# Optimization experiments

Measured on AMD Instinct MI355X. Metric: run time of the kernel, lower is better.

The kernel has to match this reference:

```python
import jax, jax.numpy as jnp
import numpy as np

B, C, N, V, W = 2, 32, 4, 32, 32
E = 256          # spa_dim
H = 8            # num_heads
D = E // H       # head_dim
K_H, K_W = 7, 7  # mask_field
EPS = 1e-5


def layer_norm(x, g, b):
    mu = jnp.mean(x, axis=-1, keepdims=True)
    var = jnp.mean(jnp.square(x - mu), axis=-1, keepdims=True)
    return (x - mu) * jax.lax.rsqrt(var + EPS) * g + b


def local_window_mask(h, w, k_h, k_w):
    # boolean [h*w, h*w]: query (i,j) attends keys (p,q) with p in [i-k_h//2, i+k_h-k_h//2), q likewise
    lh, rh = k_h // 2, k_h - k_h // 2
    lw, rw = k_w // 2, k_w - k_w // 2
    di = jnp.arange(h)[None, :] - jnp.arange(h)[:, None]   # [h(query), h(key)] = p - i
    dj = jnp.arange(w)[None, :] - jnp.arange(w)[:, None]
    mh = (di >= -lh) & (di < rh)
    mw = (dj >= -lw) & (dj < rw)
    m = mh[:, None, :, None] & mw[None, :, None, :]        # [h, w, h, w]
    return m.reshape(h * w, h * w)


def setup_inputs() -> dict:
    key = jax.random.key(0)
    ks = jax.random.split(key, 13)
    s = 0.02
    return {
        "x_lf": jax.random.normal(ks[0], (B, C, N, V, W), jnp.float32),
        "x_hf": jax.random.normal(ks[1], (B, C, N, V, W), jnp.float32),
        "w_in": jax.random.normal(ks[2], (E, C), jnp.float32) * s,       # linear_in.weight [out,in]
        "w_qk": jax.random.normal(ks[3], (E, C), jnp.float32) * s,       # linear_qk.weight
        "ln_g": jnp.ones((E,), jnp.float32),
        "ln_b": jnp.zeros((E,), jnp.float32),
        "in_proj_w": jax.random.normal(ks[4], (3 * E, E), jnp.float32) * s,
        "out_proj_w": jax.random.normal(ks[5], (E, E), jnp.float32) * s,
        "ln2_g": jnp.ones((E,), jnp.float32),
        "ln2_b": jnp.zeros((E,), jnp.float32),
        "ff_w1": jax.random.normal(ks[6], (2 * E, E), jnp.float32) * s,
        "ff_w2": jax.random.normal(ks[7], (E, 2 * E), jnp.float32) * s,
        "w_out": jax.random.normal(ks[8], (C, E), jnp.float32) * s,
    }


def reference(x_lf, x_hf, w_in, w_qk, ln_g, ln_b, in_proj_w, out_proj_w,
              ln2_g, ln2_b, ff_w1, ff_w2, w_out):
    b, c, n, v, w = x_lf.shape
    L, Bn = v * w, b * n
    mask = local_window_mask(v, w, K_H, K_W)                      # [L, L] bool

    # 'b c n v w -> (v w) (b n) c'
    tok = jnp.transpose(x_lf, (3, 4, 0, 2, 1)).reshape(L, Bn, c)
    kv = jnp.transpose(x_hf, (3, 4, 0, 2, 1)).reshape(L, Bn, c)

    epi_token = tok @ w_in.T                                       # [L, Bn, E]
    epi_kv = kv @ w_qk.T
    q_in = layer_norm(epi_token, ln_g, ln_b)
    k_in = layer_norm(epi_kv, ln_g, ln_b)
    v_in = epi_kv                                                  # value is un-normalized epi_kv

    wq, wk, wv = in_proj_w[:E], in_proj_w[E:2 * E], in_proj_w[2 * E:]
    def heads(x, wgt):
        y = x @ wgt.T                                              # [L, Bn, E]
        return jnp.transpose(y.reshape(L, Bn, H, D), (1, 2, 0, 3)) # [Bn, H, L, D]
    Q, K, Vv = heads(q_in, wq), heads(k_in, wk), heads(v_in, wv)

    scores = jnp.einsum('bhqd,bhkd->bhqk', Q, K) / jnp.sqrt(jnp.float32(D))
    scores = jnp.where(mask[None, None], scores, -jnp.inf)
    attn = jax.nn.softmax(scores, axis=-1)
    ctx = jnp.einsum('bhqk,bhkd->bhqd', attn, Vv)                  # [Bn, H, L, D]
    ctx = jnp.transpose(ctx, (2, 0, 1, 3)).reshape(L, Bn, E)
    epi_token = ctx @ out_proj_w.T + epi_token

    ff = layer_norm(epi_token, ln2_g, ln2_b)
    ff = jax.nn.relu(ff @ ff_w1.T) @ ff_w2.T
    epi_token = ff + epi_token

    out = epi_token @ w_out.T                                      # [L, Bn, C]
    # '(v w) (b n) c -> b c n v w'
    return jnp.transpose(out.reshape(v, w, b, n, c), (2, 4, 3, 0, 1))
```

## Files before the change

### kernel.cpp

```cpp
#include <hip/hip_runtime.h>
#include <hip/hip_bf16.h>


typedef __attribute__((ext_vector_type(8))) short short8v;
typedef __attribute__((ext_vector_type(4))) float f32x4;

__device__ __forceinline__ unsigned short f2bf(float x) {
    union { float f; unsigned u; } c; c.f = x;
    unsigned r = c.u + 0x7FFFu + ((c.u >> 16) & 1u);
    return (unsigned short)(r >> 16);
}
__device__ __forceinline__ float bf2f(short b) {
    union { unsigned u; float f; } c;
    c.u = ((unsigned)(unsigned short)b) << 16;
    return c.f;
}

__global__ __launch_bounds__(512) void embed_conv_kernel(
    const float* __restrict__ x_lf, const float* __restrict__ x_hf,
    const float* __restrict__ w_in, const float* __restrict__ w_qk,
    const float* __restrict__ ln_g, const float* __restrict__ ln_b,
    unsigned short* __restrict__ epi_b, unsigned short* __restrict__ kv_b,
    unsigned short* __restrict__ q_b, unsigned short* __restrict__ k_b,
    const float* __restrict__ wqkv, const float* __restrict__ wop,
    const float* __restrict__ wff1, const float* __restrict__ wff2,
    unsigned short* __restrict__ o1, unsigned short* __restrict__ o2,
    unsigned short* __restrict__ o3, unsigned short* __restrict__ o4)
{
    __shared__ float xs[2][32][36];
    __shared__ float part[2][2][2][4][4][2];

    int tid = threadIdx.x;
    int m0 = blockIdx.x * 32;
    int bn = m0 >> 10, l0 = m0 & 1023;
    int bb = bn >> 2, nn = bn & 3;

    {
        int t = tid >> 8, rem = tid & 255;
        int c = rem >> 3, i0 = (rem & 7) * 4;
        size_t base = (size_t)bb * 131072 + (size_t)c * 4096 + nn * 1024 + l0 + i0;
        const float* src = t ? x_hf : x_lf;
        *(float4*)&xs[t][c][i0] = *(const float4*)(src + base);
    }
    __syncthreads();

    int lane = tid & 63, wv = tid >> 6;
    int rA = lane & 15, k8r = lane >> 4, g = k8r, k0 = k8r * 8;
    int p = wv >> 2, rg = (wv >> 1) & 1, chh = wv & 1;
    const float* W = p ? w_qk : w_in;

    short8v afrag;
#pragma unroll
    for (int j = 0; j < 8; ++j)
        afrag[j] = (short)f2bf(xs[p][k0 + j][rg * 16 + rA]);

    f32x4 acc[8];
#pragma unroll
    for (int ct = 0; ct < 8; ++ct)
#pragma unroll
        for (int r = 0; r < 4; ++r) acc[ct][r] = 0.f;

#pragma unroll
    for (int ct = 0; ct < 8; ++ct) {
        const float* wp = W + ((chh * 8 + ct) * 16 + rA) * 32 + k0;
        float4 w0 = *(const float4*)wp;
        float4 w1 = *(const float4*)(wp + 4);
        short8v bfrag;
        bfrag[0] = (short)f2bf(w0.x); bfrag[1] = (short)f2bf(w0.y);
        bfrag[2] = (short)f2bf(w0.z); bfrag[3] = (short)f2bf(w0.w);
        bfrag[4] = (short)f2bf(w1.x); bfrag[5] = (short)f2bf(w1.y);
        bfrag[6] = (short)f2bf(w1.z); bfrag[7] = (short)f2bf(w1.w);
        acc[ct] = __builtin_amdgcn_mfma_f32_16x16x32_bf16(afrag, bfrag, acc[ct], 0, 0, 0);
    }

    float s[4] = {0.f, 0.f, 0.f, 0.f}, q[4] = {0.f, 0.f, 0.f, 0.f};
#pragma unroll
    for (int ct = 0; ct < 8; ++ct)
#pragma unroll
        for (int r = 0; r < 4; ++r) {
            float v = acc[ct][r];
            s[r] += v; q[r] += v * v;
        }
#pragma unroll
    for (int off = 8; off; off >>= 1)
#pragma unroll
        for (int r = 0; r < 4; ++r) {
            s[r] += __shfl_xor(s[r], off);
            q[r] += __shfl_xor(q[r], off);
        }
    if (rA == 0) {
#pragma unroll
        for (int r = 0; r < 4; ++r) {
            part[p][rg][chh][g][r][0] = s[r];
            part[p][rg][chh][g][r][1] = q[r];
        }
    }
    __syncthreads();
    float mu[4], rs[4];
#pragma unroll
    for (int r = 0; r < 4; ++r) {
        float S = part[p][rg][0][g][r][0] + part[p][rg][1][g][r][0];
        float Q = part[p][rg][0][g][r][1] + part[p][rg][1][g][r][1];
        mu[r] = S * (1.f / 256.f);
        rs[r] = rsqrtf(Q * (1.f / 256.f) - mu[r] * mu[r] + 1e-5f);
    }

#pragma unroll
    for (int ct = 0; ct < 8; ++ct) {
        int col = (chh * 8 + ct) * 16 + rA;
        float gg = ln_g[col], bv = ln_b[col];
#pragma unroll
        for (int r = 0; r < 4; ++r) {
            int row = m0 + rg * 16 + g * 4 + r;
            float v = acc[ct][r];
            float lnv = (v - mu[r]) * rs[r] * gg + bv;
            size_t o = (size_t)row * 256 + col;
            if (p == 0) {
                epi_b[o] = f2bf(v);
                q_b[o] = f2bf(lnv);
            } else {
                kv_b[o] = f2bf(v);
                k_b[o] = f2bf(lnv);
            }
        }
    }

    {
        int i4 = blockIdx.x * 512 + tid;
        const float* src; unsigned short* dst; int off;
        if (i4 < 49152)      { src = wqkv; dst = o1; off = i4 * 4; }
        else if (i4 < 65536) { src = wop;  dst = o2; off = (i4 - 49152) * 4; }
        else if (i4 < 98304) { src = wff1; dst = o3; off = (i4 - 65536) * 4; }
        else                 { src = wff2; dst = o4; off = (i4 - 98304) * 4; }
        float4 v = *(const float4*)(src + off);
        ushort4 u;
        u.x = f2bf(v.x); u.y = f2bf(v.y); u.z = f2bf(v.z); u.w = f2bf(v.w);
        *(ushort4*)(dst + off) = u;
    }
}

template <int OUTMAP, bool RELU>
__global__ __launch_bounds__(256) void gemm_mfma64(
    const unsigned short* __restrict__ A0, const unsigned short* __restrict__ A1,
    const unsigned short* __restrict__ A2, const unsigned short* __restrict__ Wb,
    unsigned short* __restrict__ OUT, int K, int N)
{
    int z = blockIdx.z;
    const unsigned short* A = (z == 0) ? A0 : (z == 1) ? A1 : A2;
    const unsigned short* W = Wb + (size_t)z * 65536;

    __shared__ unsigned short As[64 * 72];
    __shared__ unsigned short Ws[128 * 72];

    int tid = threadIdx.x;
    int lane = tid & 63, wid = tid >> 6;
    int wm = wid >> 1, wn = wid & 1;
    int m0 = blockIdx.x * 64, n0 = blockIdx.y * 128;

    f32x4 acc[2][4];
#pragma unroll
    for (int i = 0; i < 2; ++i)
#pragma unroll
        for (int j = 0; j < 4; ++j)
#pragma unroll
            for (int r = 0; r < 4; ++r) acc[i][j][r] = 0.f;

    int rA = lane & 15, k8r = lane >> 4, g = lane >> 4;

    for (int kc = 0; kc < K; kc += 64) {
#pragma unroll
        for (int t = 0; t < 2; ++t) {
            int idx = t * 256 + tid;
            int row = idx >> 3, k8 = idx & 7;
            *(short8v*)&As[row * 72 + k8 * 8] =
                *(const short8v*)(A + (size_t)(m0 + row) * K + kc + k8 * 8);
        }
#pragma unroll
        for (int t = 0; t < 4; ++t) {
            int idx = t * 256 + tid;
            int row = idx >> 3, k8 = idx & 7;
            *(short8v*)&Ws[row * 72 + k8 * 8] =
                *(const short8v*)(W + (size_t)(n0 + row) * K + kc + k8 * 8);
        }
        __syncthreads();

        short8v a[2][2], b[2][4];
#pragma unroll
        for (int ks = 0; ks < 2; ++ks) {
#pragma unroll
            for (int mi = 0; mi < 2; ++mi)
                a[ks][mi] = *(const short8v*)&As[(wm * 32 + mi * 16 + rA) * 72 + ks * 32 + k8r * 8];
#pragma unroll
            for (int ni = 0; ni < 4; ++ni)
                b[ks][ni] = *(const short8v*)&Ws[(wn * 64 + ni * 16 + rA) * 72 + ks * 32 + k8r * 8];
        }
#pragma unroll
        for (int ks = 0; ks < 2; ++ks)
#pragma unroll
            for (int mi = 0; mi < 2; ++mi)
#pragma unroll
                for (int ni = 0; ni < 4; ++ni)
                    acc[mi][ni] = __builtin_amdgcn_mfma_f32_16x16x32_bf16(
                        a[ks][mi], b[ks][ni], acc[mi][ni], 0, 0, 0);
        __syncthreads();
    }

#pragma unroll
    for (int mi = 0; mi < 2; ++mi) {
#pragma unroll
        for (int ni = 0; ni < 4; ++ni) {
#pragma unroll
            for (int r = 0; r < 4; ++r) {
                int row = m0 + wm * 32 + mi * 16 + g * 4 + r;
                int col = n0 + wn * 64 + ni * 16 + rA;
                float v = acc[mi][ni][r];
                if (RELU) v = fmaxf(v, 0.f);
                if (OUTMAP == 0) {
                    OUT[(size_t)row * N + col] = f2bf(v);
                } else {
                    int l = row & 1023, bn = row >> 10;
                    int h = col >> 5, d = col & 31;
                    OUT[(size_t)z * 2097152 + ((bn * 8 + h) * 1024 + l) * 32 + d] = f2bf(v);
                }
            }
        }
    }
}

__global__ __launch_bounds__(256) void attn_mfma_kernel(
    const unsigned short* __restrict__ Qb, const unsigned short* __restrict__ Kb,
    const unsigned short* __restrict__ Vb, unsigned short* __restrict__ ctx)
{
    int bh = blockIdx.x >> 5;
    int qv = blockIdx.x & 31;
    int tid = threadIdx.x, lane = tid & 63, wv = tid >> 6;
    int rA = lane & 15, k8r = lane >> 4, g = lane >> 4;

    __shared__ unsigned short KPs[7 * 32 * 40];
    __shared__ unsigned short Vt[32 * 232];
    __shared__ float redm[2][2][4][4];
    __shared__ float reds[2][2][4][4];

    unsigned short* Ks = KPs;
    unsigned short* Ps = KPs;

    int mt = wv & 1, nh = wv >> 1;

    short8v qfrag = *(const short8v*)(
        Qb + ((size_t)bh * 1024 + qv * 32 + mt * 16 + rA) * 32 + k8r * 8);

#pragma unroll
    for (int it = 0; it < 4; ++it) {
        int idx = it * 256 + tid;
        if (idx < 896) {
            int dv = idx >> 7, rem = idx & 127;
            int kw = rem >> 2, c8 = (rem & 3) * 8;
            int kvc = min(max(qv - 3 + dv, 0), 31);
            size_t base = ((size_t)bh * 1024 + kvc * 32 + kw) * 32 + c8;
            int n = dv * 32 + kw;
            *(short8v*)&Ks[n * 40 + c8] = *(const short8v*)(Kb + base);
            short8v v8 = *(const short8v*)(Vb + base);
#pragma unroll
            for (int j = 0; j < 8; ++j)
                Vt[(c8 + j) * 232 + n] = (unsigned short)v8[j];
        }
    }
    __syncthreads();

    f32x4 sc[7];
#pragma unroll
    for (int ct = 0; ct < 7; ++ct)
#pragma unroll
        for (int r = 0; r < 4; ++r) sc[ct][r] = 0.f;
#pragma unroll
    for (int ct = 0; ct < 7; ++ct) {
        short8v b = *(const short8v*)&Ks[(nh * 112 + ct * 16 + rA) * 40 + k8r * 8];
        sc[ct] = __builtin_amdgcn_mfma_f32_16x16x32_bf16(qfrag, b, sc[ct], 0, 0, 0);
    }

    const float scale = 0.17677669529663687f;
    float mx[4] = {-1e30f, -1e30f, -1e30f, -1e30f};
#pragma unroll
    for (int ct = 0; ct < 7; ++ct) {
        int n = nh * 112 + ct * 16 + rA;
        int dv = n >> 5, kw = n & 31;
        int kv = qv - 3 + dv;
        bool vv = (kv >= 0) && (kv < 32);
#pragma unroll
        for (int r = 0; r < 4; ++r) {
            int qw = mt * 16 + g * 4 + r;
            int dj = kw - qw;
            bool ok = vv && (dj >= -3) && (dj <= 3);
            float s = ok ? sc[ct][r] * scale : -1e30f;
            sc[ct][r] = s;
            mx[r] = fmaxf(mx[r], s);
        }
    }
#pragma unroll
    for (int off = 8; off; off >>= 1)
#pragma unroll
        for (int r = 0; r < 4; ++r) mx[r] = fmaxf(mx[r], __shfl_xor(mx[r], off));
    if (rA == 0) {
#pragma unroll
        for (int r = 0; r < 4; ++r) redm[mt][nh][g][r] = mx[r];
    }
    __syncthreads();
#pragma unroll
    for (int r = 0; r < 4; ++r)
        mx[r] = fmaxf(redm[mt][0][g][r], redm[mt][1][g][r]);

    float sm[4] = {0.f, 0.f, 0.f, 0.f};
#pragma unroll
    for (int ct = 0; ct < 7; ++ct)
#pragma unroll
        for (int r = 0; r < 4; ++r) {
            float e = __expf(sc[ct][r] - mx[r]);
            sc[ct][r] = e;
            sm[r] += e;
        }
#pragma unroll
    for (int off = 8; off; off >>= 1)
#pragma unroll
        for (int r = 0; r < 4; ++r) sm[r] += __shfl_xor(sm[r], off);
    if (rA == 0) {
#pragma unroll
        for (int r = 0; r < 4; ++r) reds[mt][nh][g][r] = sm[r];
    }
    __syncthreads();
    float inv[4];
#pragma unroll
    for (int r = 0; r < 4; ++r)
        inv[r] = 1.f / (reds[mt][0][g][r] + reds[mt][1][g][r]);

#pragma unroll
    for (int ct = 0; ct < 7; ++ct) {
        int n = nh * 112 + ct * 16 + rA;
#pragma unroll
        for (int r = 0; r < 4; ++r) {
            int q = mt * 16 + g * 4 + r;
            Ps[q * 232 + n] = f2bf(sc[ct][r]);
        }
    }
    __syncthreads();

    f32x4 o;
#pragma unroll
    for (int r = 0; r < 4; ++r) o[r] = 0.f;
#pragma unroll
    for (int kb = 0; kb < 7; ++kb) {
        short8v pa = *(const short8v*)&Ps[(mt * 16 + rA) * 232 + kb * 32 + k8r * 8];
        short8v vb = *(const short8v*)&Vt[(nh * 16 + rA) * 232 + kb * 32 + k8r * 8];
        o = __builtin_amdgcn_mfma_f32_16x16x32_bf16(pa, vb, o, 0, 0, 0);
    }

    {
        int bn = bh >> 3, h = bh & 7;
        int d = nh * 16 + rA;
#pragma unroll
        for (int r = 0; r < 4; ++r) {
            int q = qv * 32 + mt * 16 + g * 4 + r;
            ctx[((size_t)bn * 1024 + q) * 256 + h * 32 + d] = f2bf(o[r] * inv[r]);
        }
    }
}

__global__ __launch_bounds__(512) void outproj_ln_kernel(
    const unsigned short* __restrict__ ctx, const unsigned short* __restrict__ Wop,
    unsigned short* __restrict__ epi_b, const float* __restrict__ g2,
    const float* __restrict__ b2, unsigned short* __restrict__ ffin)
{
    __shared__ unsigned short As[32 * 72];
    __shared__ unsigned short Ws[256 * 72];
    __shared__ float part[2][4][4][4][2];

    int tid = threadIdx.x, lane = tid & 63, wv = tid >> 6;
    int m0 = blockIdx.x * 32;
    int rA = lane & 15, k8r = lane >> 4, g = lane >> 4;
    int rg = wv & 1, ch = wv >> 1;

    f32x4 acc[4];
#pragma unroll
    for (int ct = 0; ct < 4; ++ct)
#pragma unroll
        for (int r = 0; r < 4; ++r) acc[ct][r] = 0.f;

    for (int kc = 0; kc < 256; kc += 64) {
        if (tid < 256) {
            int row = tid >> 3, k8 = tid & 7;
            *(short8v*)&As[row * 72 + k8 * 8] =
                *(const short8v*)(ctx + (size_t)(m0 + row) * 256 + kc + k8 * 8);
        }
#pragma unroll
        for (int t = 0; t < 4; ++t) {
            int idx = t * 512 + tid;
            int row = idx >> 3, k8 = idx & 7;
            *(short8v*)&Ws[row * 72 + k8 * 8] =
                *(const short8v*)(Wop + (size_t)row * 256 + kc + k8 * 8);
        }
        __syncthreads();
        short8v a[2];
#pragma unroll
        for (int ks = 0; ks < 2; ++ks)
            a[ks] = *(const short8v*)&As[(rg * 16 + rA) * 72 + ks * 32 + k8r * 8];
#pragma unroll
        for (int ks = 0; ks < 2; ++ks)
#pragma unroll
            for (int ct = 0; ct < 4; ++ct) {
                short8v b = *(const short8v*)&Ws[(ch * 64 + ct * 16 + rA) * 72 + ks * 32 + k8r * 8];
                acc[ct] = __builtin_amdgcn_mfma_f32_16x16x32_bf16(a[ks], b, acc[ct], 0, 0, 0);
            }
        __syncthreads();
    }

    float s[4] = {0.f, 0.f, 0.f, 0.f}, q[4] = {0.f, 0.f, 0.f, 0.f};
#pragma unroll
    for (int ct = 0; ct < 4; ++ct) {
        int col = ch * 64 + ct * 16 + rA;
#pragma unroll
        for (int r = 0; r < 4; ++r) {
            int row = m0 + rg * 16 + g * 4 + r;
            float v = acc[ct][r] + bf2f(epi_b[(size_t)row * 256 + col]);
            acc[ct][r] = v;
            s[r] += v; q[r] += v * v;
        }
    }
#pragma unroll
    for (int off = 8; off; off >>= 1)
#pragma unroll
        for (int r = 0; r < 4; ++r) {
            s[r] += __shfl_xor(s[r], off);
            q[r] += __shfl_xor(q[r], off);
        }
    if (rA == 0) {
#pragma unroll
        for (int r = 0; r < 4; ++r) {
            part[rg][ch][g][r][0] = s[r];
            part[rg][ch][g][r][1] = q[r];
        }
    }
    __syncthreads();
    float mu[4], rs[4];
#pragma unroll
    for (int r = 0; r < 4; ++r) {
        float S = part[rg][0][g][r][0] + part[rg][1][g][r][0]
                + part[rg][2][g][r][0] + part[rg][3][g][r][0];
        float Q = part[rg][0][g][r][1] + part[rg][1][g][r][1]
                + part[rg][2][g][r][1] + part[rg][3][g][r][1];
        mu[r] = S * (1.f / 256.f);
        rs[r] = rsqrtf(Q * (1.f / 256.f) - mu[r] * mu[r] + 1e-5f);
    }
#pragma unroll
    for (int ct = 0; ct < 4; ++ct) {
        int col = ch * 64 + ct * 16 + rA;
        float gg = g2[col], bv = b2[col];
#pragma unroll
        for (int r = 0; r < 4; ++r) {
            int row = m0 + rg * 16 + g * 4 + r;
            size_t o = (size_t)row * 256 + col;
            epi_b[o] = f2bf(acc[ct][r]);
            ffin[o] = f2bf((acc[ct][r] - mu[r]) * rs[r] * gg + bv);
        }
    }
}

__global__ __launch_bounds__(512) void ff2_final_kernel(
    const unsigned short* __restrict__ ffh, const unsigned short* __restrict__ W2,
    const unsigned short* __restrict__ epi_b, const float* __restrict__ w_out,
    float* __restrict__ out)
{
    __shared__ unsigned short As[32 * 72];
    __shared__ unsigned short Ws[256 * 72];
    __shared__ unsigned short Ts[32 * 264];

    int tid = threadIdx.x, lane = tid & 63, wv = tid >> 6;
    int m0 = blockIdx.x * 32;
    int rA = lane & 15, k8r = lane >> 4, g = lane >> 4;
    int rg = wv & 1, ch = wv >> 1;

    f32x4 acc[4];
#pragma unroll
    for (int ct = 0; ct < 4; ++ct)
#pragma unroll
        for (int r = 0; r < 4; ++r) acc[ct][r] = 0.f;

    for (int kc = 0; kc < 512; kc += 64) {
        if (tid < 256) {
            int row = tid >> 3, k8 = tid & 7;
            *(short8v*)&As[row * 72 + k8 * 8] =
                *(const short8v*)(ffh + (size_t)(m0 + row) * 512 + kc + k8 * 8);
        }
#pragma unroll
        for (int t = 0; t < 4; ++t) {
            int idx = t * 512 + tid;
            int row = idx >> 3, k8 = idx & 7;
            *(short8v*)&Ws[row * 72 + k8 * 8] =
                *(const short8v*)(W2 + (size_t)row * 512 + kc + k8 * 8);
        }
        __syncthreads();
        short8v a[2];
#pragma unroll
        for (int ks = 0; ks < 2; ++ks)
            a[ks] = *(const short8v*)&As[(rg * 16 + rA) * 72 + ks * 32 + k8r * 8];
#pragma unroll
        for (int ks = 0; ks < 2; ++ks)
#pragma unroll
            for (int ct = 0; ct < 4; ++ct) {
                short8v b = *(const short8v*)&Ws[(ch * 64 + ct * 16 + rA) * 72 + ks * 32 + k8r * 8];
                acc[ct] = __builtin_amdgcn_mfma_f32_16x16x32_bf16(a[ks], b, acc[ct], 0, 0, 0);
            }
        __syncthreads();
    }

#pragma unroll
    for (int ct = 0; ct < 4; ++ct) {
        int col = ch * 64 + ct * 16 + rA;
#pragma unroll
        for (int r = 0; r < 4; ++r) {
            int lrow = rg * 16 + g * 4 + r;
            float v = acc[ct][r] + bf2f(epi_b[(size_t)(m0 + lrow) * 256 + col]);
            Ts[lrow * 264 + col] = f2bf(v);
        }
    }
    __syncthreads();

    int bn = m0 >> 10, l0 = m0 & 1023;
    int bb = bn >> 2, nn = bn & 3;

    if (wv < 4) {
        int rw = wv & 1, cw = wv >> 1;
        f32x4 a2;
#pragma unroll
        for (int r = 0; r < 4; ++r) a2[r] = 0.f;
#pragma unroll
        for (int ks = 0; ks < 8; ++ks) {
            short8v af = *(const short8v*)&Ts[(rw * 16 + rA) * 264 + ks * 32 + k8r * 8];
            const float* wp = w_out + (cw * 16 + rA) * 256 + ks * 32 + k8r * 8;
            float4 w0 = *(const float4*)wp;
            float4 w1 = *(const float4*)(wp + 4);
            short8v bf;
            bf[0] = (short)f2bf(w0.x); bf[1] = (short)f2bf(w0.y);
            bf[2] = (short)f2bf(w0.z); bf[3] = (short)f2bf(w0.w);
            bf[4] = (short)f2bf(w1.x); bf[5] = (short)f2bf(w1.y);
            bf[6] = (short)f2bf(w1.z); bf[7] = (short)f2bf(w1.w);
            a2 = __builtin_amdgcn_mfma_f32_16x16x32_bf16(af, bf, a2, 0, 0, 0);
        }
        int c = cw * 16 + rA;
        int l = l0 + rw * 16 + g * 4;
        float4 st; st.x = a2[0]; st.y = a2[1]; st.z = a2[2]; st.w = a2[3];
        *(float4*)(out + ((size_t)(bb * 32 + c) * 4 + nn) * 1024 + l) = st;
    }
}

extern "C" void kernel_launch(void* const* d_in, const int* in_sizes, int n_in,
                              void* d_out, int out_size, void* d_ws, size_t ws_size,
                              hipStream_t stream) {
    const float* x_lf       = (const float*)d_in[0];
    const float* x_hf       = (const float*)d_in[1];
    const float* w_in       = (const float*)d_in[2];
    const float* w_qk       = (const float*)d_in[3];
    const float* ln_g       = (const float*)d_in[4];
    const float* ln_b       = (const float*)d_in[5];
    const float* in_proj_w  = (const float*)d_in[6];
    const float* out_proj_w = (const float*)d_in[7];
    const float* ln2_g      = (const float*)d_in[8];
    const float* ln2_b      = (const float*)d_in[9];
    const float* ff_w1      = (const float*)d_in[10];
    const float* ff_w2      = (const float*)d_in[11];
    const float* w_out      = (const float*)d_in[12];
    float* out = (float*)d_out;

    char* w = (char*)d_ws;
    unsigned short* epi_b  = (unsigned short*)(w);
    unsigned short* Qb     = (unsigned short*)(w + (4u  << 20));
    unsigned short* Kb     = (unsigned short*)(w + (8u  << 20));
    unsigned short* Vb     = (unsigned short*)(w + (12u << 20));
    unsigned short* q_b    = (unsigned short*)(w + (16u << 20));
    unsigned short* k_b    = (unsigned short*)(w + (20u << 20));
    unsigned short* kv_b   = (unsigned short*)(w + (24u << 20));
    unsigned short* ctx_b  = (unsigned short*)(w + (28u << 20));
    unsigned short* ffin_b = (unsigned short*)(w + (32u << 20));
    unsigned short* ffh_b  = (unsigned short*)(w + (36u << 20));
    unsigned short* wqkv_b = (unsigned short*)(w + (44u << 20));
    unsigned short* wop_b  = (unsigned short*)(w + (45u << 20));
    unsigned short* wff1_b = (unsigned short*)(w + (46u << 20));
    unsigned short* wff2_b = (unsigned short*)(w + (47u << 20));

    embed_conv_kernel<<<256, 512, 0, stream>>>(
        x_lf, x_hf, w_in, w_qk, ln_g, ln_b, epi_b, kv_b, q_b, k_b,
        in_proj_w, out_proj_w, ff_w1, ff_w2, wqkv_b, wop_b, wff1_b, wff2_b);
    gemm_mfma64<1, false><<<dim3(128, 2, 3), 256, 0, stream>>>(
        q_b, k_b, kv_b, wqkv_b, Qb, 256, 256);
    attn_mfma_kernel<<<2048, 256, 0, stream>>>(Qb, Kb, Vb, ctx_b);
    outproj_ln_kernel<<<256, 512, 0, stream>>>(ctx_b, wop_b, epi_b,
                                               ln2_g, ln2_b, ffin_b);
    gemm_mfma64<0, true><<<dim3(128, 4, 1), 256, 0, stream>>>(
        ffin_b, ffin_b, ffin_b, wff1_b, ffh_b, 256, 512);
    ff2_final_kernel<<<256, 512, 0, stream>>>(ffh_b, wff2_b, epi_b, w_out, out);
}
```

Before: 73.57 us.

## Process two query rows per attention block and drop cross-wave softmax reductions

Each attention block now handles two adjacent query rows (64 queries) sharing an 8-row key/value window of 256 keys, so the grid is halved. Each wave owns 16 full query rows across all 256 keys, which lets the softmax max and sum be done with lane shuffles only and removes the shared-memory reduction barriers. The cost is more masked MFMA work per query (256 keys instead of 224) and a larger per-thread score array, which may raise register pressure.

```diff
diff --git a/kernel.cpp b/kernel.cpp
--- a/kernel.cpp
+++ b/kernel.cpp
@@ -231,66 +231,66 @@
     const unsigned short* __restrict__ Qb, const unsigned short* __restrict__ Kb,
     const unsigned short* __restrict__ Vb, unsigned short* __restrict__ ctx)
 {
-    int bh = blockIdx.x >> 5;
-    int qv = blockIdx.x & 31;
-    int tid = threadIdx.x, lane = tid & 63, wv = tid >> 6;
+    int bh = blockIdx.x >> 4;
+    int qv0 = (blockIdx.x & 15) * 2;
+    int tid = threadIdx.x, lane = tid & 63, mt = tid >> 6;
     int rA = lane & 15, k8r = lane >> 4, g = lane >> 4;
 
-    __shared__ unsigned short KPs[7 * 32 * 40];
-    __shared__ unsigned short Vt[32 * 232];
-    __shared__ float redm[2][2][4][4];
-    __shared__ float reds[2][2][4][4];
+    __shared__ unsigned short KPs[64 * 264];
+    __shared__ unsigned short Vt[32 * 264];
 
     unsigned short* Ks = KPs;
     unsigned short* Ps = KPs;
 
-    int mt = wv & 1, nh = wv >> 1;
-
-    short8v qfrag = *(const short8v*)(
-        Qb + ((size_t)bh * 1024 + qv * 32 + mt * 16 + rA) * 32 + k8r * 8);
+    short8v qfrag;
+    {
+        int qq = mt * 16 + rA;
+        int l = (qv0 + (qq >> 5)) * 32 + (qq & 31);
+        qfrag = *(const short8v*)(Qb + ((size_t)bh * 1024 + l) * 32 + k8r * 8);
+    }
 
 #pragma unroll
     for (int it = 0; it < 4; ++it) {
         int idx = it * 256 + tid;
-        if (idx < 896) {
-            int dv = idx >> 7, rem = idx & 127;
-            int kw = rem >> 2, c8 = (rem & 3) * 8;
-            int kvc = min(max(qv - 3 + dv, 0), 31);
-            size_t base = ((size_t)bh * 1024 + kvc * 32 + kw) * 32 + c8;
-            int n = dv * 32 + kw;
-            *(short8v*)&Ks[n * 40 + c8] = *(const short8v*)(Kb + base);
-            short8v v8 = *(const short8v*)(Vb + base);
-#pragma unroll
-            for (int j = 0; j < 8; ++j)
-                Vt[(c8 + j) * 232 + n] = (unsigned short)v8[j];
-        }
-    }
-    __syncthreads();
-
-    f32x4 sc[7];
-#pragma unroll
-    for (int ct = 0; ct < 7; ++ct)
+        int dv = idx >> 7, rem = idx & 127;
+        int kw = rem >> 2, c8 = (rem & 3) * 8;
+        int kvc = min(max(qv0 - 3 + dv, 0), 31);
+        size_t base = ((size_t)bh * 1024 + kvc * 32 + kw) * 32 + c8;
+        int n = dv * 32 + kw;
+        *(short8v*)&Ks[n * 40 + c8] = *(const short8v*)(Kb + base);
+        short8v v8 = *(const short8v*)(Vb + base);
+#pragma unroll
+        for (int j = 0; j < 8; ++j)
+            Vt[(c8 + j) * 264 + n] = (unsigned short)v8[j];
+    }
+    __syncthreads();
+
+    f32x4 sc[16];
+#pragma unroll
+    for (int ct = 0; ct < 16; ++ct)
 #pragma unroll
         for (int r = 0; r < 4; ++r) sc[ct][r] = 0.f;
 #pragma unroll
-    for (int ct = 0; ct < 7; ++ct) {
-        short8v b = *(const short8v*)&Ks[(nh * 112 + ct * 16 + rA) * 40 + k8r * 8];
+    for (int ct = 0; ct < 16; ++ct) {
+        short8v b = *(const short8v*)&Ks[(ct * 16 + rA) * 40 + k8r * 8];
         sc[ct] = __builtin_amdgcn_mfma_f32_16x16x32_bf16(qfrag, b, sc[ct], 0, 0, 0);
     }
+    __syncthreads();
 
     const float scale = 0.17677669529663687f;
     float mx[4] = {-1e30f, -1e30f, -1e30f, -1e30f};
 #pragma unroll
-    for (int ct = 0; ct < 7; ++ct) {
-        int n = nh * 112 + ct * 16 + rA;
+    for (int ct = 0; ct < 16; ++ct) {
+        int n = ct * 16 + rA;
         int dv = n >> 5, kw = n & 31;
-        int kv = qv - 3 + dv;
-        bool vv = (kv >= 0) && (kv < 32);
-#pragma unroll
-        for (int r = 0; r < 4; ++r) {
-            int qw = mt * 16 + g * 4 + r;
-            int dj = kw - qw;
-            bool ok = vv && (dj >= -3) && (dj <= 3);
+        int kv = qv0 - 3 + dv;
+        bool vok = (kv >= 0) && (kv < 32);
+#pragma unroll
+        for (int r = 0; r < 4; ++r) {
+            int qq = mt * 16 + g * 4 + r;
+            int v = qv0 + (qq >> 5), w = qq & 31;
+            int djv = kv - v, djw = kw - w;
+            bool ok = vok && (djv >= -3) && (djv <= 3) && (djw >= -3) && (djw <= 3);
             float s = ok ? sc[ct][r] * scale : -1e30f;
             sc[ct][r] = s;
             mx[r] = fmaxf(mx[r], s);
@@ -300,18 +300,10 @@
     for (int off = 8; off; off >>= 1)
 #pragma unroll
         for (int r = 0; r < 4; ++r) mx[r] = fmaxf(mx[r], __shfl_xor(mx[r], off));
-    if (rA == 0) {
-#pragma unroll
-        for (int r = 0; r < 4; ++r) redm[mt][nh][g][r] = mx[r];
-    }
-    __syncthreads();
-#pragma unroll
-    for (int r = 0; r < 4; ++r)
-        mx[r] = fmaxf(redm[mt][0][g][r], redm[mt][1][g][r]);
 
     float sm[4] = {0.f, 0.f, 0.f, 0.f};
 #pragma unroll
-    for (int ct = 0; ct < 7; ++ct)
+    for (int ct = 0; ct < 16; ++ct)
 #pragma unroll
         for (int r = 0; r < 4; ++r) {
             float e = __expf(sc[ct][r] - mx[r]);
@@ -322,44 +314,47 @@
     for (int off = 8; off; off >>= 1)
 #pragma unroll
         for (int r = 0; r < 4; ++r) sm[r] += __shfl_xor(sm[r], off);
-    if (rA == 0) {
-#pragma unroll
-        for (int r = 0; r < 4; ++r) reds[mt][nh][g][r] = sm[r];
-    }
-    __syncthreads();
     float inv[4];
 #pragma unroll
-    for (int r = 0; r < 4; ++r)
-        inv[r] = 1.f / (reds[mt][0][g][r] + reds[mt][1][g][r]);
-
-#pragma unroll
-    for (int ct = 0; ct < 7; ++ct) {
-        int n = nh * 112 + ct * 16 + rA;
+    for (int r = 0; r < 4; ++r) inv[r] = 1.f / sm[r];
+
+#pragma unroll
+    for (int ct = 0; ct < 16; ++ct) {
+        int n = ct * 16 + rA;
 #pragma unroll
         for (int r = 0; r < 4; ++r) {
             int q = mt * 16 + g * 4 + r;
-            Ps[q * 232 + n] = f2bf(sc[ct][r]);
-        }
-    }
-    __syncthreads();
-
-    f32x4 o;
-#pragma unroll
-    for (int r = 0; r < 4; ++r) o[r] = 0.f;
-#pragma unroll
-    for (int kb = 0; kb < 7; ++kb) {
-        short8v pa = *(const short8v*)&Ps[(mt * 16 + rA) * 232 + kb * 32 + k8r * 8];
-        short8v vb = *(const short8v*)&Vt[(nh * 16 + rA) * 232 + kb * 32 + k8r * 8];
-        o = __builtin_amdgcn_mfma_f32_16x16x32_bf16(pa, vb, o, 0, 0, 0);
+            Ps[q * 264 + n] = f2bf(sc[ct][r]);
+        }
+    }
+    __syncthreads();
+
+    f32x4 o[2];
+#pragma unroll
+    for (int dt = 0; dt < 2; ++dt)
+#pragma unroll
+        for (int r = 0; r < 4; ++r) o[dt][r] = 0.f;
+#pragma unroll
+    for (int kb = 0; kb < 8; ++kb) {
+        short8v pa = *(const short8v*)&Ps[(mt * 16 + rA) * 264 + kb * 32 + k8r * 8];
+#pragma unroll
+        for (int dt = 0; dt < 2; ++dt) {
+            short8v vb = *(const short8v*)&Vt[(dt * 16 + rA) * 264 + kb * 32 + k8r * 8];
+            o[dt] = __builtin_amdgcn_mfma_f32_16x16x32_bf16(pa, vb, o[dt], 0, 0, 0);
+        }
     }
 
     {
         int bn = bh >> 3, h = bh & 7;
-        int d = nh * 16 + rA;
-#pragma unroll
-        for (int r = 0; r < 4; ++r) {
-            int q = qv * 32 + mt * 16 + g * 4 + r;
-            ctx[((size_t)bn * 1024 + q) * 256 + h * 32 + d] = f2bf(o[r] * inv[r]);
+#pragma unroll
+        for (int dt = 0; dt < 2; ++dt) {
+            int d = dt * 16 + rA;
+#pragma unroll
+            for (int r = 0; r < 4; ++r) {
+                int qq = mt * 16 + g * 4 + r;
+                int l = (qv0 + (qq >> 5)) * 32 + (qq & 31);
+                ctx[((size_t)bn * 1024 + l) * 256 + h * 32 + d] = f2bf(o[dt][r] * inv[r]);
+            }
         }
     }
 }
@@ -590,7 +585,7 @@
         in_proj_w, out_proj_w, ff_w1, ff_w2, wqkv_b, wop_b, wff1_b, wff2_b);
     gemm_mfma64<1, false><<<dim3(128, 2, 3), 256, 0, stream>>>(
         q_b, k_b, kv_b, wqkv_b, Qb, 256, 256);
-    attn_mfma_kernel<<<2048, 256, 0, stream>>>(Qb, Kb, Vb, ctx_b);
+    attn_mfma_kernel<<<1024, 256, 0, stream>>>(Qb, Kb, Vb, ctx_b);
     outproj_ln_kernel<<<256, 512, 0, stream>>>(ctx_b, wop_b, epi_b,
                                                ln2_g, ln2_b, ffin_b);
     gemm_mfma64<0, true><<<dim3(128, 4, 1), 256, 0, stream>>>(
```

Result: faster. 67.56 us (-8.2%).
